# Kernel optimization log

Hardware: AMD Instinct MI355X
Metric: run time of the kernel (lower is better)

The kernel has to match this reference:

```python
import jax, jax.numpy as jnp
import numpy as np

N_EMBD = 512
N_HEADS = 8
N_KV_HEADS = 2
HEAD_DIM = N_EMBD // N_HEADS  # 64
ROPE_BASE = 1000000.0
B, T = 2, 4096


def _rotate_half(x):
    h = x.shape[-1] // 2
    return jnp.concatenate([-x[..., h:], x[..., :h]], axis=-1)


def _build_rope(head_dim, seq_len, base, dtype):
    inv_freq = 1.0 / base ** (jnp.arange(0, head_dim, 2, dtype=jnp.float32) / head_dim)
    t = jnp.arange(seq_len, dtype=jnp.float32)
    freqs = jnp.outer(t, inv_freq)            # [T, head_dim/2]
    emb = jnp.concatenate([freqs, freqs], axis=-1)  # [T, head_dim]
    return emb.astype(dtype), None  # placeholder, cos/sin computed by caller


def setup_inputs() -> dict:
    key = jax.random.key(0)
    ks = jax.random.split(key, 8)
    s_in = 1.0 / np.sqrt(N_EMBD)
    x = jax.random.normal(ks[0], (B, T, N_EMBD), dtype=jnp.float32)
    Wq = jax.random.normal(ks[1], (N_EMBD, N_HEADS * HEAD_DIM), dtype=jnp.float32) * s_in
    bq = jnp.zeros((N_HEADS * HEAD_DIM,), dtype=jnp.float32)
    Wk = jax.random.normal(ks[2], (N_EMBD, N_KV_HEADS * HEAD_DIM), dtype=jnp.float32) * s_in
    bk = jnp.zeros((N_KV_HEADS * HEAD_DIM,), dtype=jnp.float32)
    Wv = jax.random.normal(ks[3], (N_EMBD, N_KV_HEADS * HEAD_DIM), dtype=jnp.float32) * s_in
    bv = jnp.zeros((N_KV_HEADS * HEAD_DIM,), dtype=jnp.float32)
    Wo = jax.random.normal(ks[4], (N_HEADS * HEAD_DIM, N_EMBD), dtype=jnp.float32) * s_in
    return {"x": x, "Wq": Wq, "bq": bq, "Wk": Wk, "bk": bk, "Wv": Wv, "bv": bv, "Wo": Wo}


def reference(x, Wq, bq, Wk, bk, Wv, bv, Wo):
    Bx, Tx, _ = x.shape
    scale = HEAD_DIM ** -0.5
    q = (x @ Wq + bq).reshape(Bx, Tx, N_HEADS, HEAD_DIM).transpose(0, 2, 1, 3)      # [B,H,T,D]
    k = (x @ Wk + bk).reshape(Bx, Tx, N_KV_HEADS, HEAD_DIM).transpose(0, 2, 1, 3)   # [B,Hkv,T,D]
    v = (x @ Wv + bv).reshape(Bx, Tx, N_KV_HEADS, HEAD_DIM).transpose(0, 2, 1, 3)

    # RoPE (built in fp32 then cast, matching torch impl)
    inv_freq = 1.0 / ROPE_BASE ** (jnp.arange(0, HEAD_DIM, 2, dtype=jnp.float32) / HEAD_DIM)
    t = jnp.arange(Tx, dtype=jnp.float32)
    freqs = jnp.outer(t, inv_freq)
    emb = jnp.concatenate([freqs, freqs], axis=-1)          # [T, D]
    cos = jnp.cos(emb).astype(x.dtype)[None, None, :, :]    # broadcast over B,H
    sin = jnp.sin(emb).astype(x.dtype)[None, None, :, :]
    q = q * cos + _rotate_half(q) * sin
    k = k * cos + _rotate_half(k) * sin

    rep = N_HEADS // N_KV_HEADS
    k = jnp.repeat(k, rep, axis=1)   # repeat_interleave on head dim
    v = jnp.repeat(v, rep, axis=1)

    attn = jnp.einsum("bhtd,bhsd->bhts", q, k) * scale      # [B,H,T,T]
    causal = jnp.tril(jnp.ones((Tx, Tx), dtype=bool))
    attn = jnp.where(causal, attn, jnp.finfo(attn.dtype).min)
    attn = jax.nn.softmax(attn, axis=-1)
    out = jnp.einsum("bhts,bhsd->bhtd", attn, v)            # [B,H,T,D]
    out = out.transpose(0, 2, 1, 3).reshape(Bx, Tx, N_HEADS * HEAD_DIM)
    return out @ Wo
```

## Files before the change

kernel.cpp:

```cpp
#include <hip/hip_runtime.h>

typedef unsigned short u16;
typedef unsigned int u32;
typedef __bf16 bf16x8_t __attribute__((ext_vector_type(8)));
typedef float f32x4_t __attribute__((ext_vector_type(4)));
typedef float f32x16_t __attribute__((ext_vector_type(16)));

#define T_SEQ 4096
#define EMB 512
#define NH 8
#define NKV 2
#define HD 64

__device__ __forceinline__ float bf2f(u16 h) {
    union { unsigned u; float f; } x; x.u = ((unsigned)h) << 16; return x.f;
}
__device__ __forceinline__ u16 f2bf(float f) {
    union { float f; unsigned u; } x; x.f = f;
    unsigned r = x.u + 0x7FFFu + ((x.u >> 16) & 1u);
    return (u16)(r >> 16);
}

__global__ void transpose_kernel(const float* __restrict__ W, u16* __restrict__ WT,
                                 int K, int N) {
    int i = blockIdx.x * 256 + threadIdx.x;
    if (i < K * N) {
        int n = i / K;
        int k = i - n * K;
        WT[i] = f2bf(W[(size_t)k * N + n]);
    }
}

__global__ void cvt_kernel(const float* __restrict__ in, u16* __restrict__ out, int n4) {
    int i = blockIdx.x * 256 + threadIdx.x;
    if (i < n4) {
        float4 v = *reinterpret_cast<const float4*>(in + (size_t)i * 4);
        u16 o[4] = { f2bf(v.x), f2bf(v.y), f2bf(v.z), f2bf(v.w) };
        *reinterpret_cast<uint2*>(out + (size_t)i * 4) = *reinterpret_cast<uint2*>(o);
    }
}

__global__ void rope_table_kernel(float* __restrict__ cost, float* __restrict__ sint) {
    int i = blockIdx.x * 256 + threadIdx.x;
    int t = i >> 5, j = i & 31;
    double invf = pow(1.0e6, -(double)j / 32.0);
    double ang = (double)t * invf;
    cost[i] = (float)cos(ang);
    sint[i] = (float)sin(ang);
}

template <int EPI>
__global__ __launch_bounds__(256)
void gemm_kernel(const u16* __restrict__ A, const u16* __restrict__ Bt, int K,
                 float* __restrict__ C, int N,
                 const float* __restrict__ bq, const float* __restrict__ bk,
                 const float* __restrict__ bv,
                 const float* __restrict__ cost, const float* __restrict__ sint,
                 u16* __restrict__ qw, u16* __restrict__ kw, u16* __restrict__ vt)
{
    __shared__ __align__(16) u16 As[128][72];
    __shared__ __align__(16) u16 Bs[128][72];

    const int tid  = threadIdx.x;
    const int lane = tid & 63, wave = tid >> 6;
    const int wr = wave >> 1, wc = wave & 1;
    const int tm = blockIdx.x, tn = blockIdx.y;
    const int lrow = lane & 15, lgrp = lane >> 4;

    f32x4_t acc[4][4];
#pragma unroll
    for (int i = 0; i < 4; ++i)
#pragma unroll
        for (int j = 0; j < 4; ++j) acc[i][j] = (f32x4_t){0.f, 0.f, 0.f, 0.f};

    for (int k0 = 0; k0 < K; k0 += 64) {
        __syncthreads();
        {
            const int r0 = tid >> 3;
            const int ko = (tid & 7) * 8;
#pragma unroll
            for (int rr = 0; rr < 4; ++rr) {
                int row = r0 + rr * 32;
                uint4 va = *reinterpret_cast<const uint4*>(A + (size_t)(tm * 128 + row) * K + k0 + ko);
                *reinterpret_cast<uint4*>(&As[row][ko]) = va;
                uint4 vb = *reinterpret_cast<const uint4*>(Bt + (size_t)(tn * 128 + row) * K + k0 + ko);
                *reinterpret_cast<uint4*>(&Bs[row][ko]) = vb;
            }
        }
        __syncthreads();
#pragma unroll
        for (int kc = 0; kc < 2; ++kc) {
            bf16x8_t af[4], bf[4];
#pragma unroll
            for (int mb = 0; mb < 4; ++mb)
                af[mb] = *reinterpret_cast<const bf16x8_t*>(&As[wr * 64 + mb * 16 + lrow][kc * 32 + lgrp * 8]);
#pragma unroll
            for (int nb = 0; nb < 4; ++nb)
                bf[nb] = *reinterpret_cast<const bf16x8_t*>(&Bs[wc * 64 + nb * 16 + lrow][kc * 32 + lgrp * 8]);
#pragma unroll
            for (int mb = 0; mb < 4; ++mb)
#pragma unroll
                for (int nb = 0; nb < 4; ++nb)
                    acc[mb][nb] = __builtin_amdgcn_mfma_f32_16x16x32_bf16(af[mb], bf[nb], acc[mb][nb], 0, 0, 0);
        }
    }

    if (EPI == 0) {
#pragma unroll
        for (int mb = 0; mb < 4; ++mb)
#pragma unroll
            for (int nb = 0; nb < 4; ++nb)
#pragma unroll
                for (int r = 0; r < 4; ++r) {
                    int row = tm * 128 + wr * 64 + mb * 16 + lgrp * 4 + r;
                    int col = tn * 128 + wc * 64 + nb * 16 + lrow;
                    C[(size_t)row * N + col] = acc[mb][nb][r];
                }
    } else {
        const float QSC = 0.125f * 1.44269504088896f;
#pragma unroll
        for (int mb = 0; mb < 4; ++mb)
#pragma unroll
            for (int r = 0; r < 4; ++r) {
                int grow = tm * 128 + wr * 64 + mb * 16 + lgrp * 4 + r;
                int b = grow >> 12, t = grow & 4095;
#pragma unroll
                for (int nb = 0; nb < 2; ++nb) {
                    int n = tn * 128 + wc * 64 + nb * 16 + lrow;
                    int j = n & 63;
                    float c0 = acc[mb][nb][r];
                    float c1 = acc[mb][nb + 2][r];
                    if (n < 512) {
                        c0 += bq[n]; c1 += bq[n + 32];
                        float cs = cost[t * 32 + j], sn = sint[t * 32 + j];
                        float r0 = (c0 * cs - c1 * sn) * QSC;
                        float r1 = (c1 * cs + c0 * sn) * QSC;
                        int h = n >> 6;
                        size_t base = ((size_t)(b * NH + h) * T_SEQ + t) * HD;
                        qw[base + j]      = f2bf(r0);
                        qw[base + j + 32] = f2bf(r1);
                    } else if (n < 640) {
                        int nn = n - 512;
                        c0 += bk[nn]; c1 += bk[nn + 32];
                        float cs = cost[t * 32 + j], sn = sint[t * 32 + j];
                        float r0 = c0 * cs - c1 * sn;
                        float r1 = c1 * cs + c0 * sn;
                        int hk2 = nn >> 6;
                        size_t base = ((size_t)(b * NKV + hk2) * T_SEQ + t) * HD;
                        kw[base + j]      = f2bf(r0);
                        kw[base + j + 32] = f2bf(r1);
                    } else {
                        int nn = n - 640;
                        c0 += bv[nn]; c1 += bv[nn + 32];
                        int hv = nn >> 6;
                        size_t base = (size_t)(b * NKV + hv) * HD * T_SEQ;
                        vt[base + (size_t)j * T_SEQ + t]        = f2bf(c0);
                        vt[base + (size_t)(j + 32) * T_SEQ + t] = f2bf(c1);
                    }
                }
            }
    }
}

__global__ __launch_bounds__(256)
void attn_kernel(const u16* __restrict__ qw, const u16* __restrict__ kw,
                 const u16* __restrict__ vt, u16* __restrict__ po, float* __restrict__ lb)
{
    __shared__ __align__(16) u16 Ks[2][64][64];
    __shared__ __align__(16) u16 Vs[2][64][64];

    const int hdix = blockIdx.x;
    const int b = hdix >> 3, h = hdix & 7, hk = h >> 2;
    const int qt = 31 - (int)blockIdx.y;
    const int ck = blockIdx.z;
    const int tid = threadIdx.x, lane = tid & 63, wave = tid >> 6;
    const int lid = lane & 31, hi = lane >> 5;
    const int q0 = qt * 128 + wave * 32;
    const int kt0 = ck * (qt + 1);
    const int kt1 = kt0 + (qt + 1);

    const u16* kbase  = kw + (size_t)(b * NKV + hk) * T_SEQ * HD;
    const u16* vtbase = vt + (size_t)(b * NKV + hk) * HD * T_SEQ;

    const int ss = tid >> 3;
    const int sg = tid & 7;
    const int swz = (sg ^ (ss & 7)) << 3;

    bf16x8_t qf[4];
    {
        const u16* qrow = qw + ((size_t)(b * NH + h) * T_SEQ + q0 + lid) * HD + 8 * hi;
#pragma unroll
        for (int t = 0; t < 4; ++t)
            qf[t] = *reinterpret_cast<const bf16x8_t*>(qrow + 16 * t);
    }

    f32x16_t o0, o1;
#pragma unroll
    for (int i = 0; i < 16; ++i) { o0[i] = 0.f; o1[i] = 0.f; }
    const float M_FIX = 16.0f;
    float l = 0.f;

    {
        const int s2 = kt0 * 64;
        uint4 ka  = *reinterpret_cast<const uint4*>(kbase + (size_t)(s2 + ss) * HD + sg * 8);
        uint4 kb2 = *reinterpret_cast<const uint4*>(kbase + (size_t)(s2 + ss + 32) * HD + sg * 8);
        uint4 va  = *reinterpret_cast<const uint4*>(vtbase + (size_t)ss * T_SEQ + s2 + sg * 8);
        uint4 vb2 = *reinterpret_cast<const uint4*>(vtbase + (size_t)(ss + 32) * T_SEQ + s2 + sg * 8);
        *reinterpret_cast<uint4*>(&Ks[0][ss][swz]) = ka;
        *reinterpret_cast<uint4*>(&Ks[0][ss + 32][swz]) = kb2;
        *reinterpret_cast<uint4*>(&Vs[0][ss][swz]) = va;
        *reinterpret_cast<uint4*>(&Vs[0][ss + 32][swz]) = vb2;
    }
    __syncthreads();

    for (int kt = kt0; kt < kt1; ++kt) {
        const int cur = (kt - kt0) & 1, nxt = cur ^ 1;
        const bool pre = (kt + 1 < kt1);

        uint4 kr0, kr1, vr0, vr1;
        if (pre) {
            const int s2 = (kt + 1) * 64;
            kr0 = *reinterpret_cast<const uint4*>(kbase + (size_t)(s2 + ss) * HD + sg * 8);
            kr1 = *reinterpret_cast<const uint4*>(kbase + (size_t)(s2 + ss + 32) * HD + sg * 8);
            vr0 = *reinterpret_cast<const uint4*>(vtbase + (size_t)ss * T_SEQ + s2 + sg * 8);
            vr1 = *reinterpret_cast<const uint4*>(vtbase + (size_t)(ss + 32) * T_SEQ + s2 + sg * 8);
        }

        if (kt * 64 <= q0 + 31) {
            const bool full = (kt * 64 + 32 <= q0 + 31);
            const bool mreq = (kt * 64 + 63 > q0);

            f32x16_t s0, s1;
#pragma unroll
            for (int i = 0; i < 16; ++i) { s0[i] = 0.f; s1[i] = 0.f; }
            __builtin_amdgcn_s_setprio(1);
#pragma unroll
            for (int t = 0; t < 4; ++t) {
                const int g = ((2 * t + hi) ^ (lid & 7)) << 3;
                bf16x8_t ka = *reinterpret_cast<const bf16x8_t*>(&Ks[cur][lid][g]);
                s0 = __builtin_amdgcn_mfma_f32_32x32x16_bf16(ka, qf[t], s0, 0, 0, 0);
                if (full) {
                    bf16x8_t kb2 = *reinterpret_cast<const bf16x8_t*>(&Ks[cur][lid + 32][g]);
                    s1 = __builtin_amdgcn_mfma_f32_32x32x16_bf16(kb2, qf[t], s1, 0, 0, 0);
                }
            }
            __builtin_amdgcn_s_setprio(0);

            if (mreq) {
                const int qg = q0 + lid;
                const int kvb = kt * 64 + 4 * hi;
#pragma unroll
                for (int r = 0; r < 16; ++r) {
                    int kv = kvb + (r & 3) + 8 * (r >> 2);
                    if (kv > qg) s0[r] = -1e30f;
                    if (full && kv + 32 > qg) s1[r] = -1e30f;
                }
            }

#pragma unroll
            for (int r = 0; r < 16; ++r) s0[r] = exp2f(s0[r] - M_FIX);
            if (full) {
#pragma unroll
                for (int r = 0; r < 16; ++r) s1[r] = exp2f(s1[r] - M_FIX);
            }

            {
                float rs = 0.f;
#pragma unroll
                for (int q4 = 0; q4 < 4; ++q4)
                    rs += (s0[4 * q4] + s0[4 * q4 + 1]) + (s0[4 * q4 + 2] + s0[4 * q4 + 3]);
                if (full) {
#pragma unroll
                    for (int q4 = 0; q4 < 4; ++q4)
                        rs += (s1[4 * q4] + s1[4 * q4 + 1]) + (s1[4 * q4 + 2] + s1[4 * q4 + 3]);
                }
                rs += __shfl_xor(rs, 32);
                l += rs;
            }

            bf16x8_t pa[4];
            {
                u32 pw[8], pe[8];
                uint4 f0, f1;
#pragma unroll
                for (int c = 0; c < 4; ++c) {
                    asm("v_cvt_pk_bf16_f32 %0, %1, %2" : "=v"(pw[2 * c])     : "v"(s0[4 * c]),     "v"(s0[4 * c + 1]));
                    asm("v_cvt_pk_bf16_f32 %0, %1, %2" : "=v"(pw[2 * c + 1]) : "v"(s0[4 * c + 2]), "v"(s0[4 * c + 3]));
                }
#pragma unroll
                for (int i = 0; i < 8; ++i) pe[i] = (u32)__shfl_xor((int)pw[i], 32);
                f0.x = hi ? pe[2] : pw[0]; f0.y = hi ? pe[3] : pw[1];
                f0.z = hi ? pw[2] : pe[0]; f0.w = hi ? pw[3] : pe[1];
                f1.x = hi ? pe[6] : pw[4]; f1.y = hi ? pe[7] : pw[5];
                f1.z = hi ? pw[6] : pe[4]; f1.w = hi ? pw[7] : pe[5];
                pa[0] = __builtin_bit_cast(bf16x8_t, f0);
                pa[1] = __builtin_bit_cast(bf16x8_t, f1);
                if (full) {
#pragma unroll
                    for (int c = 0; c < 4; ++c) {
                        asm("v_cvt_pk_bf16_f32 %0, %1, %2" : "=v"(pw[2 * c])     : "v"(s1[4 * c]),     "v"(s1[4 * c + 1]));
                        asm("v_cvt_pk_bf16_f32 %0, %1, %2" : "=v"(pw[2 * c + 1]) : "v"(s1[4 * c + 2]), "v"(s1[4 * c + 3]));
                    }
#pragma unroll
                    for (int i = 0; i < 8; ++i) pe[i] = (u32)__shfl_xor((int)pw[i], 32);
                    f0.x = hi ? pe[2] : pw[0]; f0.y = hi ? pe[3] : pw[1];
                    f0.z = hi ? pw[2] : pe[0]; f0.w = hi ? pw[3] : pe[1];
                    f1.x = hi ? pe[6] : pw[4]; f1.y = hi ? pe[7] : pw[5];
                    f1.z = hi ? pw[6] : pe[4]; f1.w = hi ? pw[7] : pe[5];
                    pa[2] = __builtin_bit_cast(bf16x8_t, f0);
                    pa[3] = __builtin_bit_cast(bf16x8_t, f1);
                }
            }

            __builtin_amdgcn_s_setprio(1);
            const int ns = full ? 4 : 2;
#pragma unroll
            for (int s = 0; s < 4; ++s) {
                if (s >= ns) break;
                const int g = ((2 * s + hi) ^ (lid & 7)) << 3;
                bf16x8_t v0f = *reinterpret_cast<const bf16x8_t*>(&Vs[cur][lid][g]);
                bf16x8_t v1f = *reinterpret_cast<const bf16x8_t*>(&Vs[cur][lid + 32][g]);
                o0 = __builtin_amdgcn_mfma_f32_32x32x16_bf16(pa[s], v0f, o0, 0, 0, 0);
                o1 = __builtin_amdgcn_mfma_f32_32x32x16_bf16(pa[s], v1f, o1, 0, 0, 0);
            }
            __builtin_amdgcn_s_setprio(0);
        }

        if (pre) {
            *reinterpret_cast<uint4*>(&Ks[nxt][ss][swz]) = kr0;
            *reinterpret_cast<uint4*>(&Ks[nxt][ss + 32][swz]) = kr1;
            *reinterpret_cast<uint4*>(&Vs[nxt][ss][swz]) = vr0;
            *reinterpret_cast<uint4*>(&Vs[nxt][ss + 32][swz]) = vr1;
            __syncthreads();
        }
    }

    {
        const int bq = (hdix * 32 + qt) * 128;
        u16* pob = po + (size_t)ck * 8388608 / 2 * 2;
        pob = po + (size_t)ck * 4194304;
#pragma unroll
        for (int r = 0; r < 16; ++r) {
            int qr = (r & 3) + 8 * (r >> 2) + 4 * hi;
            size_t base = (size_t)(bq + wave * 32 + qr) * HD;
            pob[base + lid]      = f2bf(o0[r]);
            pob[base + lid + 32] = f2bf(o1[r]);
        }
        if (hi == 0)
            lb[(size_t)ck * 65536 + bq + wave * 32 + lid] = l;
    }
}

__global__ __launch_bounds__(256)
void combine_kernel(const u16* __restrict__ po, const float* __restrict__ lb,
                    u16* __restrict__ ao)
{
    int id = blockIdx.x * 256 + threadIdx.x;
    int row = id >> 3, oct = id & 3 + (id & 7) - (id & 3);
    oct = id & 7;
    int bhqt = row >> 7, qrow = row & 127;
    int bh = bhqt >> 5, qt = bhqt & 31;
    int b = bh >> 3, h = bh & 7;
    int t = qt * 128 + qrow;

    float inv = 1.0f / (lb[row] + lb[65536 + row]);
    const u16* p0 = po + (size_t)row * HD + oct * 8;
    const u16* p1 = p0 + 4194304;
    uint4 a = *reinterpret_cast<const uint4*>(p0);
    uint4 c = *reinterpret_cast<const uint4*>(p1);
    const u16* pa = reinterpret_cast<const u16*>(&a);
    const u16* pc = reinterpret_cast<const u16*>(&c);
    u16 outv[8];
#pragma unroll
    for (int j = 0; j < 8; ++j)
        outv[j] = f2bf((bf2f(pa[j]) + bf2f(pc[j])) * inv);
    size_t base = ((size_t)(b * T_SEQ) + t) * EMB + h * HD + oct * 8;
    *reinterpret_cast<uint2*>(ao + base)     = *reinterpret_cast<uint2*>(&outv[0]);
    *reinterpret_cast<uint2*>(ao + base + 4) = *reinterpret_cast<uint2*>(&outv[4]);
}

extern "C" void kernel_launch(void* const* d_in, const int* in_sizes, int n_in,
                              void* d_out, int out_size, void* d_ws, size_t ws_size,
                              hipStream_t stream)
{
    const float* x  = (const float*)d_in[0];
    const float* Wq = (const float*)d_in[1];
    const float* bq = (const float*)d_in[2];
    const float* Wk = (const float*)d_in[3];
    const float* bk = (const float*)d_in[4];
    const float* Wv = (const float*)d_in[5];
    const float* bv = (const float*)d_in[6];
    const float* Wo = (const float*)d_in[7];
    float* out = (float*)d_out;

    char* ws = (char*)d_ws;
    u16*   WqkvT = (u16*)(ws);
    u16*   WoT   = (u16*)(ws + 786432);
    float* cost  = (float*)(ws + 1310720);
    float* sint  = (float*)(ws + 1835008);
    u16*   xbf   = (u16*)(ws + 2359296);
    u16*   qw    = (u16*)(ws + 10747904);
    u16*   kw    = (u16*)(ws + 19136512);
    u16*   vt    = (u16*)(ws + 21233664);
    u16*   ao    = (u16*)(ws + 23330816);
    u16*   po    = xbf;
    u16*   po1   = (u16*)(ws + 31719424);
    float* lb    = (float*)(ws + 40108032);
    (void)po1;
    po = (u16*)(ws + 31719424);
    lb = (float*)(ws + 48497664);

    transpose_kernel<<<(512 * 512 + 255) / 256, 256, 0, stream>>>(Wq, WqkvT, 512, 512);
    transpose_kernel<<<(512 * 128 + 255) / 256, 256, 0, stream>>>(Wk, WqkvT + 512 * 512, 512, 128);
    transpose_kernel<<<(512 * 128 + 255) / 256, 256, 0, stream>>>(Wv, WqkvT + 640 * 512, 512, 128);
    transpose_kernel<<<(512 * 512 + 255) / 256, 256, 0, stream>>>(Wo, WoT, 512, 512);
    cvt_kernel<<<(2 * T_SEQ * EMB / 4 + 255) / 256, 256, 0, stream>>>(x, xbf, 2 * T_SEQ * EMB / 4);
    rope_table_kernel<<<(T_SEQ * 32) / 256, 256, 0, stream>>>(cost, sint);

    dim3 gp(64, 6);
    gemm_kernel<1><<<gp, 256, 0, stream>>>(xbf, WqkvT, 512, nullptr, 768,
                                           bq, bk, bv, cost, sint, qw, kw, vt);

    dim3 ga(2 * NH, 32, 2);
    attn_kernel<<<ga, 256, 0, stream>>>(qw, kw, vt, po, lb);

    combine_kernel<<<65536 * 8 / 256, 256, 0, stream>>>(po, lb, ao);

    dim3 go(64, 4);
    gemm_kernel<0><<<go, 256, 0, stream>>>(ao, WoT, 512, out, 512,
                                           nullptr, nullptr, nullptr, nullptr, nullptr,
                                           nullptr, nullptr, nullptr);
}
```

Before: 148.3 us.

## Balance causal attention split-K with variable chunk counts per query tile

Replaces the fixed two-way key split per query tile with a 1D grid. Each query tile is cut into up to three chunks of at most 22 key tiles, so the longest blocks get shorter and the work per block is more even. The combine kernel now sums a variable number of partial outputs and row sums, and the first partial buffer reuses the bf16 x buffer. It adds a small decode loop per block and extra partial-buffer traffic for long tiles.

```diff
diff --git a/kernel.cpp b/kernel.cpp
--- a/kernel.cpp
+++ b/kernel.cpp
@@ -164,20 +164,30 @@
 
 __global__ __launch_bounds__(256)
 void attn_kernel(const u16* __restrict__ qw, const u16* __restrict__ kw,
-                 const u16* __restrict__ vt, u16* __restrict__ po, float* __restrict__ lb)
+                 const u16* __restrict__ vt, u16* __restrict__ po0,
+                 u16* __restrict__ po12, float* __restrict__ lb)
 {
     __shared__ __align__(16) u16 Ks[2][64][64];
     __shared__ __align__(16) u16 Vs[2][64][64];
 
-    const int hdix = blockIdx.x;
-    const int b = hdix >> 3, h = hdix & 7, hk = h >> 2;
-    const int qt = 31 - (int)blockIdx.y;
-    const int ck = blockIdx.z;
+    int gid = blockIdx.x;
+    int qt = 31, nt, nc;
+    for (;;) {
+        nt = 2 * qt + 2;
+        nc = (nt + 21) / 22;
+        int g = nc * 16;
+        if (gid < g) break;
+        gid -= g; --qt;
+    }
+    const int bh = gid / nc;
+    const int ck = gid - bh * nc;
+    const int b = bh >> 3, h = bh & 7, hk = h >> 2;
+    const int kt0 = ck * nt / nc;
+    const int kt1 = (ck + 1) * nt / nc;
+
     const int tid = threadIdx.x, lane = tid & 63, wave = tid >> 6;
     const int lid = lane & 31, hi = lane >> 5;
     const int q0 = qt * 128 + wave * 32;
-    const int kt0 = ck * (qt + 1);
-    const int kt1 = kt0 + (qt + 1);
 
     const u16* kbase  = kw + (size_t)(b * NKV + hk) * T_SEQ * HD;
     const u16* vtbase = vt + (size_t)(b * NKV + hk) * HD * T_SEQ;
@@ -336,44 +346,60 @@
     }
 
     {
-        const int bq = (hdix * 32 + qt) * 128;
-        u16* pob = po + (size_t)ck * 8388608 / 2 * 2;
-        pob = po + (size_t)ck * 4194304;
+        u16* pob = (ck == 0) ? po0 : (po12 + (size_t)(ck - 1) * 4194304);
+        const int rowb = (bh * 32 + qt) * 128 + wave * 32;
 #pragma unroll
         for (int r = 0; r < 16; ++r) {
             int qr = (r & 3) + 8 * (r >> 2) + 4 * hi;
-            size_t base = (size_t)(bq + wave * 32 + qr) * HD;
+            size_t base = (size_t)(rowb + qr) * HD;
             pob[base + lid]      = f2bf(o0[r]);
             pob[base + lid + 32] = f2bf(o1[r]);
         }
         if (hi == 0)
-            lb[(size_t)ck * 65536 + bq + wave * 32 + lid] = l;
+            lb[(size_t)ck * 65536 + rowb + lid] = l;
     }
 }
 
 __global__ __launch_bounds__(256)
-void combine_kernel(const u16* __restrict__ po, const float* __restrict__ lb,
-                    u16* __restrict__ ao)
+void combine_kernel(const u16* __restrict__ po0, const u16* __restrict__ po12,
+                    const float* __restrict__ lb, u16* __restrict__ ao)
 {
     int id = blockIdx.x * 256 + threadIdx.x;
-    int row = id >> 3, oct = id & 3 + (id & 7) - (id & 3);
-    oct = id & 7;
+    int row = id >> 3, oct = id & 7;
     int bhqt = row >> 7, qrow = row & 127;
     int bh = bhqt >> 5, qt = bhqt & 31;
     int b = bh >> 3, h = bh & 7;
     int t = qt * 128 + qrow;
-
-    float inv = 1.0f / (lb[row] + lb[65536 + row]);
-    const u16* p0 = po + (size_t)row * HD + oct * 8;
-    const u16* p1 = p0 + 4194304;
-    uint4 a = *reinterpret_cast<const uint4*>(p0);
-    uint4 c = *reinterpret_cast<const uint4*>(p1);
-    const u16* pa = reinterpret_cast<const u16*>(&a);
-    const u16* pc = reinterpret_cast<const u16*>(&c);
+    int nc = (2 * qt + 2 + 21) / 22;
+
+    float lsum = lb[row];
+    if (nc > 1) lsum += lb[65536 + row];
+    if (nc > 2) lsum += lb[131072 + row];
+    float inv = 1.0f / lsum;
+
+    float acc[8];
+    {
+        uint4 a = *reinterpret_cast<const uint4*>(po0 + (size_t)row * HD + oct * 8);
+        const u16* pa = reinterpret_cast<const u16*>(&a);
+#pragma unroll
+        for (int j = 0; j < 8; ++j) acc[j] = bf2f(pa[j]);
+    }
+    if (nc > 1) {
+        uint4 a = *reinterpret_cast<const uint4*>(po12 + (size_t)row * HD + oct * 8);
+        const u16* pa = reinterpret_cast<const u16*>(&a);
+#pragma unroll
+        for (int j = 0; j < 8; ++j) acc[j] += bf2f(pa[j]);
+    }
+    if (nc > 2) {
+        uint4 a = *reinterpret_cast<const uint4*>(po12 + 4194304 + (size_t)row * HD + oct * 8);
+        const u16* pa = reinterpret_cast<const u16*>(&a);
+#pragma unroll
+        for (int j = 0; j < 8; ++j) acc[j] += bf2f(pa[j]);
+    }
+
     u16 outv[8];
 #pragma unroll
-    for (int j = 0; j < 8; ++j)
-        outv[j] = f2bf((bf2f(pa[j]) + bf2f(pc[j])) * inv);
+    for (int j = 0; j < 8; ++j) outv[j] = f2bf(acc[j] * inv);
     size_t base = ((size_t)(b * T_SEQ) + t) * EMB + h * HD + oct * 8;
     *reinterpret_cast<uint2*>(ao + base)     = *reinterpret_cast<uint2*>(&outv[0]);
     *reinterpret_cast<uint2*>(ao + base + 4) = *reinterpret_cast<uint2*>(&outv[4]);
@@ -403,12 +429,9 @@
     u16*   kw    = (u16*)(ws + 19136512);
     u16*   vt    = (u16*)(ws + 21233664);
     u16*   ao    = (u16*)(ws + 23330816);
-    u16*   po    = xbf;
-    u16*   po1   = (u16*)(ws + 31719424);
-    float* lb    = (float*)(ws + 40108032);
-    (void)po1;
-    po = (u16*)(ws + 31719424);
-    lb = (float*)(ws + 48497664);
+    u16*   po0   = xbf;
+    u16*   po12  = (u16*)(ws + 31719424);
+    float* lb    = (float*)(ws + 48496640);
 
     transpose_kernel<<<(512 * 512 + 255) / 256, 256, 0, stream>>>(Wq, WqkvT, 512, 512);
     transpose_kernel<<<(512 * 128 + 255) / 256, 256, 0, stream>>>(Wk, WqkvT + 512 * 512, 512, 128);
@@ -421,10 +444,9 @@
     gemm_kernel<1><<<gp, 256, 0, stream>>>(xbf, WqkvT, 512, nullptr, 768,
                                            bq, bk, bv, cost, sint, qw, kw, vt);
 
-    dim3 ga(2 * NH, 32, 2);
-    attn_kernel<<<ga, 256, 0, stream>>>(qw, kw, vt, po, lb);
-
-    combine_kernel<<<65536 * 8 / 256, 256, 0, stream>>>(po, lb, ao);
+    attn_kernel<<<1008, 256, 0, stream>>>(qw, kw, vt, po0, po12, lb);
+
+    combine_kernel<<<65536 * 8 / 256, 256, 0, stream>>>(po0, po12, lb, ao);
 
     dim3 go(64, 4);
     gemm_kernel<0><<<go, 256, 0, stream>>>(ao, WoT, 512, out, 512,
```

New measurement: 161.3 us. +8.7%, slower.
